# Kernel tuning notes

Hardware: AMD Instinct MI355X
Metric: run time of the kernel (lower is better)

Reference implementation:

```python
import jax, jax.numpy as jnp
import numpy as np

N_NODES = 50000
IN_DIM = 256
OUT_DIM = 128
NNZ_FEAT = 800000
NNZ_ADJ = 800000


def setup_inputs() -> dict:
    key = jax.random.key(0)
    ks = jax.random.split(key, 10)
    inp = {
        "feat_row": jax.random.randint(ks[0], (NNZ_FEAT,), 0, N_NODES, dtype=jnp.int32),
        "feat_col": jax.random.randint(ks[1], (NNZ_FEAT,), 0, IN_DIM, dtype=jnp.int32),
        "feat_vals": jnp.ones((NNZ_FEAT,), dtype=jnp.float32),  # binary features (int-cast in original)
        "adj1_row": jax.random.randint(ks[2], (NNZ_ADJ,), 0, N_NODES, dtype=jnp.int32),
        "adj1_col": jax.random.randint(ks[3], (NNZ_ADJ,), 0, N_NODES, dtype=jnp.int32),
        "adj1_vals": jax.random.uniform(ks[4], (NNZ_ADJ,), dtype=jnp.float32),
        "adj2_row": jax.random.randint(ks[5], (NNZ_ADJ,), 0, N_NODES, dtype=jnp.int32),
        "adj2_col": jax.random.randint(ks[6], (NNZ_ADJ,), 0, N_NODES, dtype=jnp.int32),
        "adj2_vals": jax.random.uniform(ks[7], (NNZ_ADJ,), dtype=jnp.float32),
    }
    # Glorot-uniform weights as in weight_variable_glorot
    lim = np.sqrt(6.0 / (IN_DIM + OUT_DIM))
    inp["W1"] = jax.random.uniform(ks[8], (IN_DIM, OUT_DIM), minval=-lim, maxval=lim, dtype=jnp.float32)
    inp["W2"] = jax.random.uniform(ks[9], (IN_DIM, OUT_DIM), minval=-lim, maxval=lim, dtype=jnp.float32)
    inp["n_nodes"] = N_NODES
    return inp


def _spmm_feat(row, col, vals, W, n_nodes):
    # X (sparse [N, F]) @ W ([F, D]) -> [N, D]
    msg = vals[:, None] * W[col]  # [nnz, D]
    return jax.ops.segment_sum(msg, row, num_segments=n_nodes)


def _spmm_adj(row, col, vals, H, n_nodes):
    # A (sparse [N, N]) @ H ([N, D]) -> [N, D]
    msg = vals[:, None] * H[col]  # [E, D]
    return jax.ops.segment_sum(msg, row, num_segments=n_nodes)


def reference(feat_row, feat_col, feat_vals, adj1_row, adj1_col, adj1_vals,
              adj2_row, adj2_col, adj2_vals, W1, W2, n_nodes):
    # dropout=0.0 -> keep_prob=1 -> sparse dropout is identity with scale 1.0
    xw1 = _spmm_feat(feat_row, feat_col, feat_vals, W1, n_nodes)   # [N, D]
    x1 = _spmm_adj(adj1_row, adj1_col, adj1_vals, xw1, n_nodes)    # [N, D]
    xw2 = _spmm_feat(feat_row, feat_col, feat_vals, W2, n_nodes)
    x2 = _spmm_adj(adj2_row, adj2_col, adj2_vals, xw2, n_nodes)
    return jax.nn.relu(x1 + x2)
```

## Files before the change

kernel.cpp:

```cpp
#include <hip/hip_runtime.h>
#include <hip/hip_fp16.h>

#define N_NODES 50000
#define IN_DIM 256
#define OUT_DIM 128
#define NNZ 800000
#define SCAN_N (3 * N_NODES)
#define TOTAL_NNZ (3 * NNZ)
#define NPART 8
#define PART_W (N_NODES / NPART)

#define BCAP 310016

#define NSUB 64
#define SUBW 98
#define SUBCAP 6144
#define ENT_B 4096
#define BBLK_B ((BCAP + ENT_B - 1) / ENT_B)

#define ADJ_SL 4
#define ADJ_RC ((N_NODES + 63) / 64)

typedef float vf4 __attribute__((ext_vector_type(4)));

static __device__ __forceinline__ unsigned pack_cv(int c, float v) {
    return ((unsigned)c << 16) | (unsigned)__half_as_ushort(__float2half(v));
}
static __device__ __forceinline__ int   upk_c(unsigned pk) { return (int)(pk >> 16); }
static __device__ __forceinline__ float upk_v(unsigned pk) {
    return __half2float(__ushort_as_half((unsigned short)(pk & 0xffffu)));
}
static __device__ __forceinline__ float h2f(unsigned short h) {
    return __half2float(__ushort_as_half(h));
}
static __device__ __forceinline__ unsigned pk2h(float x, float y) {
    return (unsigned)__half_as_ushort(__float2half(x))
         | ((unsigned)__half_as_ushort(__float2half(y)) << 16);
}

__global__ void wprep_kernel(const float* __restrict__ W1,
                             const float* __restrict__ W2,
                             uint4* __restrict__ Wc) {
    int idx = blockIdx.x * 256 + threadIdx.x;
    const float4* w1 = (const float4*)W1;
    const float4* w2 = (const float4*)W2;
    float4 a = w1[idx];
    float4 b = w2[idx];
    uint4 o;
    o.x = pk2h(a.x, a.y);
    o.y = pk2h(a.z, a.w);
    o.z = pk2h(b.x, b.y);
    o.w = pk2h(b.z, b.w);
    Wc[idx] = o;
}

__global__ void bucket_kernel(const int* __restrict__ fr, const int* __restrict__ fc,
                              const float* __restrict__ fv,
                              const int* __restrict__ a1r, const int* __restrict__ a1c,
                              const float* __restrict__ a1v,
                              const int* __restrict__ a2r, const int* __restrict__ a2c,
                              const float* __restrict__ a2v,
                              int* __restrict__ bcur,
                              unsigned* __restrict__ gpack,
                              unsigned short* __restrict__ gmeta) {
    __shared__ int cnt8[8];
    __shared__ int offc[8];
    __shared__ int gbase[8];
    __shared__ unsigned spk[768];
    __shared__ unsigned short smeta[768];
    int t = threadIdx.x;
    if (t < 8) cnt8[t] = 0;
    __syncthreads();

    int e = blockIdx.x * 256 + t;
    int r[3]; unsigned pk[3]; int loc[3]; int pb[3];
    r[0] = __builtin_nontemporal_load(&fr[e]);
    pk[0] = pack_cv(__builtin_nontemporal_load(&fc[e]),
                    __builtin_nontemporal_load(&fv[e]));
    r[1] = __builtin_nontemporal_load(&a1r[e]);
    pk[1] = pack_cv(__builtin_nontemporal_load(&a1c[e]),
                    __builtin_nontemporal_load(&a1v[e]));
    r[2] = __builtin_nontemporal_load(&a2r[e]);
    pk[2] = pack_cv(__builtin_nontemporal_load(&a2c[e]),
                    __builtin_nontemporal_load(&a2v[e]));
#pragma unroll
    for (int s = 0; s < 3; ++s) {
        pb[s] = r[s] / PART_W;
        loc[s] = atomicAdd(&cnt8[pb[s]], 1);
    }
    __syncthreads();
    if (t < 8) gbase[t] = atomicAdd(&bcur[t], cnt8[t]);
    if (t == 0) {
        int acc = 0;
#pragma unroll
        for (int q = 0; q < 8; ++q) { offc[q] = acc; acc += cnt8[q]; }
    }
    __syncthreads();
#pragma unroll
    for (int s = 0; s < 3; ++s) {
        int pos = offc[pb[s]] + loc[s];
        spk[pos] = pk[s];
        smeta[pos] = (unsigned short)((s << 13) | (r[s] - pb[s] * PART_W));
    }
    __syncthreads();
#pragma unroll
    for (int k = 0; k < 3; ++k) {
        int i = t + k * 256;
        int q = 0;
#pragma unroll
        for (int b = 1; b < 8; ++b) q += (i >= offc[b]);
        int g = q * BCAP + gbase[q] + (i - offc[q]);
        gpack[g] = spk[i];
        gmeta[g] = smeta[i];
    }
}

__global__ void subbucket_kernel(const unsigned* __restrict__ gpack1,
                                 const unsigned short* __restrict__ gmeta1,
                                 const int* __restrict__ bcur,
                                 int* __restrict__ subcur,
                                 unsigned* __restrict__ gpack2,
                                 unsigned short* __restrict__ gmeta2) {
    int p = blockIdx.x & (NPART - 1);
    int chunk = blockIdx.x >> 3;
    int base = chunk * ENT_B;
    int n = bcur[p];
    int cnt = n - base;
    if (cnt <= 0) return;
    if (cnt > ENT_B) cnt = ENT_B;
    __shared__ int c64[NSUB];
    __shared__ int off[NSUB];
    __shared__ int gb[NSUB];
    __shared__ unsigned spk[ENT_B];
    __shared__ unsigned short smt[ENT_B];
    int t = threadIdx.x;
    if (t < NSUB) c64[t] = 0;
    __syncthreads();
    unsigned pk[16]; unsigned short mt[16]; int loc[16]; int sb[16];
#pragma unroll
    for (int k = 0; k < 16; ++k) {
        int i = t + k * 256;
        if (i < cnt) {
            pk[k] = gpack1[p * BCAP + base + i];
            mt[k] = gmeta1[p * BCAP + base + i];
            sb[k] = (int)(mt[k] & 8191u) / SUBW;
            loc[k] = atomicAdd(&c64[sb[k]], 1);
        } else sb[k] = -1;
    }
    __syncthreads();
    if (t == 0) {
        int a = 0;
#pragma unroll
        for (int q = 0; q < NSUB; ++q) { off[q] = a; a += c64[q]; }
    }
    __syncthreads();
    if (t < NSUB && c64[t] > 0) gb[t] = atomicAdd(&subcur[p * NSUB + t], c64[t]);
    __syncthreads();
#pragma unroll
    for (int k = 0; k < 16; ++k) {
        if (sb[k] >= 0) {
            int pos = off[sb[k]] + loc[k];
            spk[pos] = pk[k];
            smt[pos] = mt[k];
        }
    }
    __syncthreads();
    for (int i = t; i < cnt; i += 256) {
        unsigned short m = smt[i];
        int s2 = (int)(m & 8191u) / SUBW;
        int g = (p * NSUB + s2) * SUBCAP + gb[s2] + (i - off[s2]);
        gpack2[g] = spk[i];
        gmeta2[g] = m;
    }
}

__global__ __launch_bounds__(512) void sort_write_kernel(
        const unsigned* __restrict__ gpack2,
        const unsigned short* __restrict__ gmeta2,
        const int* __restrict__ subcur,
        int* __restrict__ cur3,
        int* __restrict__ starts,
        int* __restrict__ rowlen,
        unsigned* __restrict__ spack) {
    int p = blockIdx.x & (NPART - 1);
    int sub = blockIdx.x >> 3;
    int n = subcur[p * NSUB + sub];
    __shared__ int h[512];
    __shared__ int e[512];
    __shared__ int cur[512];
    __shared__ int segbase[4];
    __shared__ int gbs[3];
    __shared__ unsigned sorted[SUBCAP];
    int t = threadIdx.x;
    h[t] = 0;
    __syncthreads();
    long base = (long)(p * NSUB + sub) * SUBCAP;
    unsigned pk[12]; short ky[12];
#pragma unroll
    for (int k = 0; k < 12; ++k) {
        int i = t + k * 512;
        if (i < n) {
            pk[k] = gpack2[base + i];
            unsigned short m = gmeta2[base + i];
            int key = (int)(m >> 13) * SUBW + ((int)(m & 8191u) - sub * SUBW);
            ky[k] = (short)key;
            atomicAdd(&h[key], 1);
        } else ky[k] = -1;
    }
    __syncthreads();
    e[t] = h[t];
    __syncthreads();
    for (int off = 1; off < 512; off <<= 1) {
        int v = (t >= off) ? e[t - off] : 0;
        __syncthreads();
        e[t] += v;
        __syncthreads();
    }
    int excl = e[t] - h[t];
    __syncthreads();
    e[t] = excl;
    cur[t] = excl;
    __syncthreads();
    if (t == 0) {
        segbase[0] = 0;
        segbase[1] = e[SUBW];
        segbase[2] = e[2 * SUBW];
        segbase[3] = n;
    }
    __syncthreads();
    if (t < 3) gbs[t] = atomicAdd(&cur3[t], segbase[t + 1] - segbase[t]);
#pragma unroll
    for (int k = 0; k < 12; ++k) {
        if (ky[k] >= 0) {
            int pos = atomicAdd(&cur[ky[k]], 1);
            sorted[pos] = pk[k];
        }
    }
    __syncthreads();
    if (t < 3 * SUBW) {
        int s = t / SUBW, d = t - s * SUBW;
        int rl = sub * SUBW + d;
        if (rl < PART_W) {
            int gr = s * N_NODES + p * PART_W + rl;
            starts[gr] = s * NNZ + gbs[s] + (e[t] - segbase[s]);
            rowlen[gr] = h[t];
        }
    }
    int s1 = segbase[1], s2 = segbase[2];
#pragma unroll
    for (int k = 0; k < 12; ++k) {
        int i = t + k * 512;
        if (i < n) {
            int sg = (i < s1) ? 0 : ((i < s2) ? 1 : 2);
            spack[sg * NNZ + gbs[sg] + (i - segbase[sg])] = sorted[i];
        }
    }
}

__global__ void feat_gather_kernel(const int* __restrict__ starts,
                                   const int* __restrict__ rowlen,
                                   const unsigned* __restrict__ spack,
                                   const uint4* __restrict__ Wc,
                                   ushort4* __restrict__ xw1s,
                                   ushort4* __restrict__ xw2s) {
    int lane = threadIdx.x & 31;
    int sub  = threadIdx.x >> 5;
    int r = blockIdx.x * 8 + sub;
    if (r >= N_NODES) return;
    int s = starts[r];
    int e = s + rowlen[r];
    float4 a1 = make_float4(0.f, 0.f, 0.f, 0.f);
    float4 a2 = make_float4(0.f, 0.f, 0.f, 0.f);
    for (int base = s; base < e; base += 32) {
        int n = e - base;
        int m = (n < 32) ? n : 32;
        unsigned pk = (lane < m) ? spack[base + lane] : 0u;
        int j = 0;
        for (; j + 7 < m; j += 8) {
            unsigned pp[8]; uint4 wv[8];
#pragma unroll
            for (int k = 0; k < 8; ++k) pp[k] = __shfl(pk, j + k, 32);
#pragma unroll
            for (int k = 0; k < 8; ++k) wv[k] = Wc[upk_c(pp[k]) * 32 + lane];
#pragma unroll
            for (int k = 0; k < 8; ++k) {
                float v = upk_v(pp[k]);
                a1.x += v * h2f((unsigned short)(wv[k].x & 0xffffu));
                a1.y += v * h2f((unsigned short)(wv[k].x >> 16));
                a1.z += v * h2f((unsigned short)(wv[k].y & 0xffffu));
                a1.w += v * h2f((unsigned short)(wv[k].y >> 16));
                a2.x += v * h2f((unsigned short)(wv[k].z & 0xffffu));
                a2.y += v * h2f((unsigned short)(wv[k].z >> 16));
                a2.z += v * h2f((unsigned short)(wv[k].w & 0xffffu));
                a2.w += v * h2f((unsigned short)(wv[k].w >> 16));
            }
        }
        for (; j < m; ++j) {
            unsigned pj = __shfl(pk, j, 32);
            float v = upk_v(pj);
            uint4 wv = Wc[upk_c(pj) * 32 + lane];
            a1.x += v * h2f((unsigned short)(wv.x & 0xffffu));
            a1.y += v * h2f((unsigned short)(wv.x >> 16));
            a1.z += v * h2f((unsigned short)(wv.y & 0xffffu));
            a1.w += v * h2f((unsigned short)(wv.y >> 16));
            a2.x += v * h2f((unsigned short)(wv.z & 0xffffu));
            a2.y += v * h2f((unsigned short)(wv.z >> 16));
            a2.z += v * h2f((unsigned short)(wv.w & 0xffffu));
            a2.w += v * h2f((unsigned short)(wv.w >> 16));
        }
    }
    ushort4 q1, q2;
    q1.x = __half_as_ushort(__float2half(a1.x)); q1.y = __half_as_ushort(__float2half(a1.y));
    q1.z = __half_as_ushort(__float2half(a1.z)); q1.w = __half_as_ushort(__float2half(a1.w));
    q2.x = __half_as_ushort(__float2half(a2.x)); q2.y = __half_as_ushort(__float2half(a2.y));
    q2.z = __half_as_ushort(__float2half(a2.z)); q2.w = __half_as_ushort(__float2half(a2.w));
    size_t idx = (size_t)(lane >> 3) * (N_NODES * 8) + (size_t)r * 8 + (lane & 7);
    xw1s[idx] = q1;
    xw2s[idx] = q2;
}

__global__ __launch_bounds__(512) void adj_pass_fused(
        const int* __restrict__ starts,
        const int* __restrict__ rowlen,
        const unsigned* __restrict__ spack,
        const ushort4* __restrict__ xw1s,
        const ushort4* __restrict__ xw2s,
        vf4* __restrict__ out) {
    int s  = blockIdx.x & (ADJ_SL - 1);
    int rc = blockIdx.x >> 2;
    int g  = threadIdx.x >> 3;
    int q  = threadIdx.x & 7;
    int r  = rc * 64 + g;
    bool valid = (r < N_NODES);
    vf4 acc = {0.f, 0.f, 0.f, 0.f};

#pragma unroll
    for (int rel = 0; rel < 2; ++rel) {
        const ushort4* __restrict__ sl =
            ((rel == 0) ? xw1s : xw2s) + (size_t)s * (N_NODES * 8);
        int st = 0, en = 0;
        if (valid) {
            st = starts[(1 + rel) * N_NODES + r];
            en = st + rowlen[(1 + rel) * N_NODES + r];
        }
        for (int base = st; base < en; base += 16) {
            int m = en - base;
            unsigned pk0 = (q < m)     ? spack[base + q]     : 0u;
            unsigned pk1 = (8 + q < m) ? spack[base + 8 + q] : 0u;
            {
                unsigned pp[8]; ushort4 xx[8];
#pragma unroll
                for (int k = 0; k < 8; ++k) pp[k] = __shfl(pk0, k, 8);
#pragma unroll
                for (int k = 0; k < 8; ++k) xx[k] = sl[upk_c(pp[k]) * 8 + q];
#pragma unroll
                for (int k = 0; k < 8; ++k) {
                    float v = upk_v(pp[k]);
                    acc.x += v * h2f(xx[k].x); acc.y += v * h2f(xx[k].y);
                    acc.z += v * h2f(xx[k].z); acc.w += v * h2f(xx[k].w);
                }
            }
            if (m <= 8) continue;
            {
                unsigned pp[8]; ushort4 xx[8];
#pragma unroll
                for (int k = 0; k < 8; ++k) pp[k] = __shfl(pk1, k, 8);
#pragma unroll
                for (int k = 0; k < 8; ++k) xx[k] = sl[upk_c(pp[k]) * 8 + q];
#pragma unroll
                for (int k = 0; k < 8; ++k) {
                    float v = upk_v(pp[k]);
                    acc.x += v * h2f(xx[k].x); acc.y += v * h2f(xx[k].y);
                    acc.z += v * h2f(xx[k].z); acc.w += v * h2f(xx[k].w);
                }
            }
        }
    }
    if (valid) {
        vf4 res;
        res.x = fmaxf(acc.x, 0.f);
        res.y = fmaxf(acc.y, 0.f);
        res.z = fmaxf(acc.z, 0.f);
        res.w = fmaxf(acc.w, 0.f);
        __builtin_nontemporal_store(res, &out[(size_t)r * 32 + s * 8 + q]);
    }
}

extern "C" void kernel_launch(void* const* d_in, const int* in_sizes, int n_in,
                              void* d_out, int out_size, void* d_ws, size_t ws_size,
                              hipStream_t stream) {
    const int*   feat_row  = (const int*)  d_in[0];
    const int*   feat_col  = (const int*)  d_in[1];
    const float* feat_vals = (const float*)d_in[2];
    const int*   adj1_row  = (const int*)  d_in[3];
    const int*   adj1_col  = (const int*)  d_in[4];
    const float* adj1_vals = (const float*)d_in[5];
    const int*   adj2_row  = (const int*)  d_in[6];
    const int*   adj2_col  = (const int*)  d_in[7];
    const float* adj2_vals = (const float*)d_in[8];
    const float* W1        = (const float*)d_in[9];
    const float* W2        = (const float*)d_in[10];

    char* ws = (char*)d_ws;
    unsigned* spack = (unsigned*)ws;            ws += (size_t)TOTAL_NNZ * 4;
    int*      starts= (int*)ws;                 ws += (size_t)SCAN_N * 4;
    int*      rowlen= (int*)ws;                 ws += (size_t)SCAN_N * 4;
    int*      bcur  = (int*)ws;                 ws += 16 * 4;
    int*      subcur= (int*)ws;                 ws += (size_t)NPART * NSUB * 4;
    int*      cur3  = (int*)ws;                 ws += 16 * 4;
    uint4*    Wc    = (uint4*)ws;               ws += (size_t)256 * 32 * 16;
    char*     bkt   = ws;
    unsigned* gpack1 = (unsigned*)bkt;
    unsigned short* gmeta1 = (unsigned short*)(bkt + (size_t)NPART * BCAP * 4);
    unsigned* gpack2 = (unsigned*)(bkt + (size_t)NPART * BCAP * 6);
    unsigned short* gmeta2 = (unsigned short*)(bkt + (size_t)NPART * BCAP * 6
                                                  + (size_t)NPART * NSUB * SUBCAP * 4);
    ushort4*  xw1s  = (ushort4*)bkt;
    ushort4*  xw2s  = (ushort4*)(bkt + (size_t)N_NODES * OUT_DIM * 2);

    (void)hipMemsetAsync(bcur, 0, (16 + NPART * NSUB + 16) * sizeof(int), stream);

    const int block = 256;

    wprep_kernel<<<32, block, 0, stream>>>(W1, W2, Wc);

    bucket_kernel<<<NNZ / block, block, 0, stream>>>(
        feat_row, feat_col, feat_vals,
        adj1_row, adj1_col, adj1_vals,
        adj2_row, adj2_col, adj2_vals,
        bcur, gpack1, gmeta1);

    subbucket_kernel<<<NPART * BBLK_B, block, 0, stream>>>(
        gpack1, gmeta1, bcur, subcur, gpack2, gmeta2);

    sort_write_kernel<<<NPART * NSUB, 512, 0, stream>>>(
        gpack2, gmeta2, subcur, cur3, starts, rowlen, spack);

    const int grid_rows = N_NODES / 8;
    feat_gather_kernel<<<grid_rows, 256, 0, stream>>>(
        starts, rowlen, spack, Wc, xw1s, xw2s);

    adj_pass_fused<<<ADJ_SL * ADJ_RC, 512, 0, stream>>>(
        starts, rowlen, spack, xw1s, xw2s, (vf4*)d_out);
}
```

Measured before the change: 251.0 us.

## Merge two-level bucketing into a single 511-way superbucket scatter pass

Replaces the 8-way partition kernel and the following 64-way subbucket kernel with one kernel that scatters COO entries straight into 511 row-range buckets. It uses a block-local 512-entry histogram and a prefix scan in shared memory, and stores the local sort key in the meta field. This removes one full global write/read round trip of the packed entries and one launch. In exchange each block does a wider scan and writes scattered output into 511 destinations, so global write coalescing is weaker.

```diff
diff --git a/kernel.cpp b/kernel.cpp
--- a/kernel.cpp
+++ b/kernel.cpp
@@ -7,16 +7,13 @@
 #define NNZ 800000
 #define SCAN_N (3 * N_NODES)
 #define TOTAL_NNZ (3 * NNZ)
-#define NPART 8
-#define PART_W (N_NODES / NPART)
-
-#define BCAP 310016
-
-#define NSUB 64
+
+#define NSB 511
 #define SUBW 98
 #define SUBCAP 6144
-#define ENT_B 4096
-#define BBLK_B ((BCAP + ENT_B - 1) / ENT_B)
+
+#define EB 1024
+#define SB_GRID ((NNZ + EB - 1) / EB)
 
 #define ADJ_SL 4
 #define ADJ_RC ((N_NODES + 63) / 64)
@@ -54,123 +51,85 @@
     Wc[idx] = o;
 }
 
-__global__ void bucket_kernel(const int* __restrict__ fr, const int* __restrict__ fc,
-                              const float* __restrict__ fv,
-                              const int* __restrict__ a1r, const int* __restrict__ a1c,
-                              const float* __restrict__ a1v,
-                              const int* __restrict__ a2r, const int* __restrict__ a2c,
-                              const float* __restrict__ a2v,
-                              int* __restrict__ bcur,
-                              unsigned* __restrict__ gpack,
-                              unsigned short* __restrict__ gmeta) {
-    __shared__ int cnt8[8];
-    __shared__ int offc[8];
-    __shared__ int gbase[8];
-    __shared__ unsigned spk[768];
-    __shared__ unsigned short smeta[768];
+__global__ __launch_bounds__(512) void superbucket_kernel(
+        const int* __restrict__ fr, const int* __restrict__ fc,
+        const float* __restrict__ fv,
+        const int* __restrict__ a1r, const int* __restrict__ a1c,
+        const float* __restrict__ a1v,
+        const int* __restrict__ a2r, const int* __restrict__ a2c,
+        const float* __restrict__ a2v,
+        int* __restrict__ subcur,
+        unsigned* __restrict__ gpack2,
+        unsigned short* __restrict__ gmeta2) {
+    __shared__ unsigned long long stage[3 * EB];
+    __shared__ int c512[512];
+    __shared__ int offE[512];
+    __shared__ int gb[512];
     int t = threadIdx.x;
-    if (t < 8) cnt8[t] = 0;
-    __syncthreads();
-
-    int e = blockIdx.x * 256 + t;
-    int r[3]; unsigned pk[3]; int loc[3]; int pb[3];
-    r[0] = __builtin_nontemporal_load(&fr[e]);
-    pk[0] = pack_cv(__builtin_nontemporal_load(&fc[e]),
-                    __builtin_nontemporal_load(&fv[e]));
-    r[1] = __builtin_nontemporal_load(&a1r[e]);
-    pk[1] = pack_cv(__builtin_nontemporal_load(&a1c[e]),
-                    __builtin_nontemporal_load(&a1v[e]));
-    r[2] = __builtin_nontemporal_load(&a2r[e]);
-    pk[2] = pack_cv(__builtin_nontemporal_load(&a2c[e]),
-                    __builtin_nontemporal_load(&a2v[e]));
-#pragma unroll
-    for (int s = 0; s < 3; ++s) {
-        pb[s] = r[s] / PART_W;
-        loc[s] = atomicAdd(&cnt8[pb[s]], 1);
-    }
-    __syncthreads();
-    if (t < 8) gbase[t] = atomicAdd(&bcur[t], cnt8[t]);
-    if (t == 0) {
-        int acc = 0;
-#pragma unroll
-        for (int q = 0; q < 8; ++q) { offc[q] = acc; acc += cnt8[q]; }
-    }
-    __syncthreads();
-#pragma unroll
-    for (int s = 0; s < 3; ++s) {
-        int pos = offc[pb[s]] + loc[s];
-        spk[pos] = pk[s];
-        smeta[pos] = (unsigned short)((s << 13) | (r[s] - pb[s] * PART_W));
-    }
-    __syncthreads();
-#pragma unroll
-    for (int k = 0; k < 3; ++k) {
-        int i = t + k * 256;
-        int q = 0;
-#pragma unroll
-        for (int b = 1; b < 8; ++b) q += (i >= offc[b]);
-        int g = q * BCAP + gbase[q] + (i - offc[q]);
-        gpack[g] = spk[i];
-        gmeta[g] = smeta[i];
-    }
-}
-
-__global__ void subbucket_kernel(const unsigned* __restrict__ gpack1,
-                                 const unsigned short* __restrict__ gmeta1,
-                                 const int* __restrict__ bcur,
-                                 int* __restrict__ subcur,
-                                 unsigned* __restrict__ gpack2,
-                                 unsigned short* __restrict__ gmeta2) {
-    int p = blockIdx.x & (NPART - 1);
-    int chunk = blockIdx.x >> 3;
-    int base = chunk * ENT_B;
-    int n = bcur[p];
-    int cnt = n - base;
-    if (cnt <= 0) return;
-    if (cnt > ENT_B) cnt = ENT_B;
-    __shared__ int c64[NSUB];
-    __shared__ int off[NSUB];
-    __shared__ int gb[NSUB];
-    __shared__ unsigned spk[ENT_B];
-    __shared__ unsigned short smt[ENT_B];
-    int t = threadIdx.x;
-    if (t < NSUB) c64[t] = 0;
-    __syncthreads();
-    unsigned pk[16]; unsigned short mt[16]; int loc[16]; int sb[16];
-#pragma unroll
-    for (int k = 0; k < 16; ++k) {
-        int i = t + k * 256;
-        if (i < cnt) {
-            pk[k] = gpack1[p * BCAP + base + i];
-            mt[k] = gmeta1[p * BCAP + base + i];
-            sb[k] = (int)(mt[k] & 8191u) / SUBW;
-            loc[k] = atomicAdd(&c64[sb[k]], 1);
-        } else sb[k] = -1;
-    }
-    __syncthreads();
-    if (t == 0) {
-        int a = 0;
-#pragma unroll
-        for (int q = 0; q < NSUB; ++q) { off[q] = a; a += c64[q]; }
-    }
-    __syncthreads();
-    if (t < NSUB && c64[t] > 0) gb[t] = atomicAdd(&subcur[p * NSUB + t], c64[t]);
-    __syncthreads();
-#pragma unroll
-    for (int k = 0; k < 16; ++k) {
-        if (sb[k] >= 0) {
-            int pos = off[sb[k]] + loc[k];
-            spk[pos] = pk[k];
-            smt[pos] = mt[k];
-        }
-    }
-    __syncthreads();
-    for (int i = t; i < cnt; i += 256) {
-        unsigned short m = smt[i];
-        int s2 = (int)(m & 8191u) / SUBW;
-        int g = (p * NSUB + s2) * SUBCAP + gb[s2] + (i - off[s2]);
-        gpack2[g] = spk[i];
-        gmeta2[g] = m;
+    c512[t] = 0;
+    __syncthreads();
+    int base = blockIdx.x * EB;
+    int nE = NNZ - base; if (nE > EB) nE = EB;
+    int tot = 3 * nE;
+
+    unsigned long long ent[6]; int sbA[6]; int loc[6];
+#pragma unroll
+    for (int k = 0; k < 2; ++k) {
+        int i = k * 512 + t;
+        int e = base + i;
+        if (i < nE) {
+            int r0 = __builtin_nontemporal_load(&fr[e]);
+            unsigned p0 = pack_cv(__builtin_nontemporal_load(&fc[e]),
+                                  __builtin_nontemporal_load(&fv[e]));
+            int s0 = r0 / SUBW;
+            ent[3*k]   = ((unsigned long long)s0 << 48)
+                       | ((unsigned long long)(r0 - s0 * SUBW) << 32) | p0;
+            sbA[3*k] = s0;  loc[3*k] = atomicAdd(&c512[s0], 1);
+
+            int r1 = __builtin_nontemporal_load(&a1r[e]);
+            unsigned p1 = pack_cv(__builtin_nontemporal_load(&a1c[e]),
+                                  __builtin_nontemporal_load(&a1v[e]));
+            int s1 = r1 / SUBW;
+            ent[3*k+1] = ((unsigned long long)s1 << 48)
+                       | ((unsigned long long)(SUBW + r1 - s1 * SUBW) << 32) | p1;
+            sbA[3*k+1] = s1;  loc[3*k+1] = atomicAdd(&c512[s1], 1);
+
+            int r2 = __builtin_nontemporal_load(&a2r[e]);
+            unsigned p2 = pack_cv(__builtin_nontemporal_load(&a2c[e]),
+                                  __builtin_nontemporal_load(&a2v[e]));
+            int s2 = r2 / SUBW;
+            ent[3*k+2] = ((unsigned long long)s2 << 48)
+                       | ((unsigned long long)(2 * SUBW + r2 - s2 * SUBW) << 32) | p2;
+            sbA[3*k+2] = s2;  loc[3*k+2] = atomicAdd(&c512[s2], 1);
+        } else {
+            sbA[3*k] = sbA[3*k+1] = sbA[3*k+2] = -1;
+        }
+    }
+    __syncthreads();
+    offE[t] = c512[t];
+    __syncthreads();
+    for (int off = 1; off < 512; off <<= 1) {
+        int v = (t >= off) ? offE[t - off] : 0;
+        __syncthreads();
+        offE[t] += v;
+        __syncthreads();
+    }
+    int excl = offE[t] - c512[t];
+    __syncthreads();
+    offE[t] = excl;
+    if (c512[t] > 0) gb[t] = atomicAdd(&subcur[t], c512[t]);
+    __syncthreads();
+#pragma unroll
+    for (int k = 0; k < 6; ++k) {
+        if (sbA[k] >= 0) stage[offE[sbA[k]] + loc[k]] = ent[k];
+    }
+    __syncthreads();
+    for (int i = t; i < tot; i += 512) {
+        unsigned long long v = stage[i];
+        int sb = (int)(v >> 48);
+        int g = sb * SUBCAP + gb[sb] + (i - offE[sb]);
+        gpack2[g] = (unsigned)v;
+        gmeta2[g] = (unsigned short)(v >> 32);
     }
 }
 
@@ -182,9 +141,8 @@
         int* __restrict__ starts,
         int* __restrict__ rowlen,
         unsigned* __restrict__ spack) {
-    int p = blockIdx.x & (NPART - 1);
-    int sub = blockIdx.x >> 3;
-    int n = subcur[p * NSUB + sub];
+    int sb = blockIdx.x;
+    int n = subcur[sb];
     __shared__ int h[512];
     __shared__ int e[512];
     __shared__ int cur[512];
@@ -194,17 +152,15 @@
     int t = threadIdx.x;
     h[t] = 0;
     __syncthreads();
-    long base = (long)(p * NSUB + sub) * SUBCAP;
+    long base = (long)sb * SUBCAP;
     unsigned pk[12]; short ky[12];
 #pragma unroll
     for (int k = 0; k < 12; ++k) {
         int i = t + k * 512;
         if (i < n) {
             pk[k] = gpack2[base + i];
-            unsigned short m = gmeta2[base + i];
-            int key = (int)(m >> 13) * SUBW + ((int)(m & 8191u) - sub * SUBW);
-            ky[k] = (short)key;
-            atomicAdd(&h[key], 1);
+            ky[k] = (short)gmeta2[base + i];
+            atomicAdd(&h[ky[k]], 1);
         } else ky[k] = -1;
     }
     __syncthreads();
@@ -239,9 +195,9 @@
     __syncthreads();
     if (t < 3 * SUBW) {
         int s = t / SUBW, d = t - s * SUBW;
-        int rl = sub * SUBW + d;
-        if (rl < PART_W) {
-            int gr = s * N_NODES + p * PART_W + rl;
+        int r = sb * SUBW + d;
+        if (r < N_NODES) {
+            int gr = s * N_NODES + r;
             starts[gr] = s * NNZ + gbs[s] + (e[t] - segbase[s]);
             rowlen[gr] = h[t];
         }
@@ -405,35 +361,26 @@
     unsigned* spack = (unsigned*)ws;            ws += (size_t)TOTAL_NNZ * 4;
     int*      starts= (int*)ws;                 ws += (size_t)SCAN_N * 4;
     int*      rowlen= (int*)ws;                 ws += (size_t)SCAN_N * 4;
-    int*      bcur  = (int*)ws;                 ws += 16 * 4;
-    int*      subcur= (int*)ws;                 ws += (size_t)NPART * NSUB * 4;
+    int*      subcur= (int*)ws;                 ws += 512 * 4;
     int*      cur3  = (int*)ws;                 ws += 16 * 4;
     uint4*    Wc    = (uint4*)ws;               ws += (size_t)256 * 32 * 16;
     char*     bkt   = ws;
-    unsigned* gpack1 = (unsigned*)bkt;
-    unsigned short* gmeta1 = (unsigned short*)(bkt + (size_t)NPART * BCAP * 4);
-    unsigned* gpack2 = (unsigned*)(bkt + (size_t)NPART * BCAP * 6);
-    unsigned short* gmeta2 = (unsigned short*)(bkt + (size_t)NPART * BCAP * 6
-                                                  + (size_t)NPART * NSUB * SUBCAP * 4);
+    unsigned* gpack2 = (unsigned*)bkt;
+    unsigned short* gmeta2 = (unsigned short*)(bkt + (size_t)NSB * SUBCAP * 4);
     ushort4*  xw1s  = (ushort4*)bkt;
     ushort4*  xw2s  = (ushort4*)(bkt + (size_t)N_NODES * OUT_DIM * 2);
 
-    (void)hipMemsetAsync(bcur, 0, (16 + NPART * NSUB + 16) * sizeof(int), stream);
-
-    const int block = 256;
-
-    wprep_kernel<<<32, block, 0, stream>>>(W1, W2, Wc);
-
-    bucket_kernel<<<NNZ / block, block, 0, stream>>>(
+    (void)hipMemsetAsync(subcur, 0, (512 + 16) * sizeof(int), stream);
+
+    wprep_kernel<<<32, 256, 0, stream>>>(W1, W2, Wc);
+
+    superbucket_kernel<<<SB_GRID, 512, 0, stream>>>(
         feat_row, feat_col, feat_vals,
         adj1_row, adj1_col, adj1_vals,
         adj2_row, adj2_col, adj2_vals,
-        bcur, gpack1, gmeta1);
-
-    subbucket_kernel<<<NPART * BBLK_B, block, 0, stream>>>(
-        gpack1, gmeta1, bcur, subcur, gpack2, gmeta2);
-
-    sort_write_kernel<<<NPART * NSUB, 512, 0, stream>>>(
+        subcur, gpack2, gmeta2);
+
+    sort_write_kernel<<<NSB, 512, 0, stream>>>(
         gpack2, gmeta2, subcur, cur3, starts, rowlen, spack);
 
     const int grid_rows = N_NODES / 8;
```

Result: faster. 223.8 us (-10.8%).
